# Performance work log

Measured on AMD Instinct MI355X. Metric: run time of the kernel, lower is better.

## Reference

```python
import jax, jax.numpy as jnp
import numpy as np

B, S, V, P = 16, 100, 50000, 45
WE, PE, H = 100, 50, 400
H2 = 2 * H  # bilstm output size


def _lstm(x, Wih, Whh, b):
    """Unidirectional LSTM over time. x: [B,S,D] -> h: [B,S,H]. PyTorch gate order i,f,g,o."""
    Hs = Whh.shape[1]
    def step(carry, xt):
        h, c = carry
        g = xt @ Wih.T + h @ Whh.T + b
        i, f, gg, o = jnp.split(g, 4, axis=-1)
        c = jax.nn.sigmoid(f) * c + jax.nn.sigmoid(i) * jnp.tanh(gg)
        h = jax.nn.sigmoid(o) * jnp.tanh(c)
        return (h, c), h
    Bn = x.shape[0]
    init = (jnp.zeros((Bn, Hs), x.dtype), jnp.zeros((Bn, Hs), x.dtype))
    _, hs = jax.lax.scan(step, init, jnp.swapaxes(x, 0, 1))
    return jnp.swapaxes(hs, 0, 1)


def _bilstm_layer(x, Wf_ih, Wf_hh, bf, Wb_ih, Wb_hh, bb):
    hf = _lstm(x, Wf_ih, Wf_hh, bf)
    hb = _lstm(x[:, ::-1, :], Wb_ih, Wb_hh, bb)[:, ::-1, :]
    return jnp.concatenate([hf, hb], axis=-1)


def setup_inputs() -> dict:
    key = jax.random.key(0)
    ks = jax.random.split(key, 24)
    def n(k, shape, s=0.1):
        return jax.random.normal(k, shape, jnp.float32) * s
    inp = {
        "input_tokens": jax.random.randint(ks[0], (B, S), 0, V),
        "input_pos": jax.random.randint(ks[1], (B, S), 0, P),
        "input_head": jax.random.randint(ks[2], (B, S), 0, S),
        "word_W": n(ks[3], (V, WE)),
        "pos_W": n(ks[4], (P, PE)),
        "l0f_Wih": n(ks[5], (4 * H, WE + PE)), "l0f_Whh": n(ks[6], (4 * H, H)), "l0f_b": n(ks[7], (4 * H,)),
        "l0b_Wih": n(ks[8], (4 * H, WE + PE)), "l0b_Whh": n(ks[9], (4 * H, H)), "l0b_b": n(ks[10], (4 * H,)),
        "l1f_Wih": n(ks[11], (4 * H, H2)), "l1f_Whh": n(ks[12], (4 * H, H)), "l1f_b": n(ks[13], (4 * H,)),
        "l1b_Wih": n(ks[14], (4 * H, H2)), "l1b_Whh": n(ks[15], (4 * H, H)), "l1b_b": n(ks[16], (4 * H,)),
        "ua_W": n(ks[17], (H2, H2)), "ua_b": n(ks[18], (H2,)),
        "wa_W": n(ks[19], (H2, H2)), "wa_b": n(ks[20], (H2,)),
        "va_W": n(ks[21], (H2,)),
    }
    return inp


def reference(input_tokens, input_pos, input_head, word_W, pos_W,
              l0f_Wih, l0f_Whh, l0f_b, l0b_Wih, l0b_Whh, l0b_b,
              l1f_Wih, l1f_Whh, l1f_b, l1b_Wih, l1b_Whh, l1b_b,
              ua_W, ua_b, wa_W, wa_b, va_W):
    # embeddings (dropout is identity at eval)
    x = jnp.concatenate([word_W[input_tokens], pos_W[input_pos]], axis=-1)  # [B,S,150]
    h1 = _bilstm_layer(x, l0f_Wih, l0f_Whh, l0f_b, l0b_Wih, l0b_Whh, l0b_b)   # [B,S,H2]
    out = _bilstm_layer(h1, l1f_Wih, l1f_Whh, l1f_b, l1b_Wih, l1b_Whh, l1b_b)  # [B,S,H2]

    # batched additive biaffine scoring for targets i = 1..S-1 over all source positions j
    ua = out @ ua_W.T + ua_b  # u_a(source)  [B,S,H2]
    wa = out @ wa_W.T + wa_b  # w_a(target)  [B,S,H2]
    # g[b,t,j] = v_a . tanh(ua[b,j] + wa[b,t+1])
    g = jnp.einsum('btjh,h->btj', jnp.tanh(ua[:, None, :, :] + wa[:, 1:, None, :]), va_W)  # [B,S-1,S]
    # mask: output[:, j, 0] == output[:, i, 0]  (masks self, matching torch's output.eq(target)[:,:,0])
    mask = out[:, 1:, 0][:, :, None] == out[:, :, 0][:, None, :]  # [B,S-1,S]
    g = jnp.where(mask, -10000.0, g)
    logp = jax.nn.log_softmax(g, axis=2)  # log_softmax over source positions (torch dim=1)

    # loss: sum over i of NLLLoss(mean over batch, ignore_index=-1)
    gold = input_head[:, 1:]  # [B,S-1]
    valid = (gold != -1)
    nll = -jnp.take_along_axis(logp, jnp.clip(gold, 0, S - 1)[:, :, None], axis=2)[..., 0]
    nll = nll * valid.astype(logp.dtype)
    denom = jnp.maximum(valid.sum(axis=0), 1).astype(logp.dtype)
    loss = jnp.sum(nll.sum(axis=0) / denom)

    parent_prob_table = jnp.exp(logp)  # [B,S-1,S]
    preds = jnp.argmax(parent_prob_table, axis=2)  # [B,S-1]
    return (loss, preds, parent_prob_table)
```

## Files before the change

kernel.cpp:

```cpp
#include <hip/hip_runtime.h>

#define BB 16
#define SS 100
#define HH 400
#define H2 800
#define G4 1600
#define DIN0 150
#define KP0 160

#define OFF_X0   0ULL
#define OFF_GF   240000ULL
#define OFF_GB   2800000ULL
#define OFF_H1   5360000ULL
#define OFF_OUT2 6640000ULL
#define OFF_SC   7920000ULL
#define OFF_NLL  8078400ULL
#define OFF_CNT  8080000ULL
#define OFF_EXH  8081600ULL
#define EX_U16_PER_PLANE 1331200ULL

#define PAD_X0   0ULL
#define PAD_WF   256000ULL
#define PAD_WB   512000ULL

typedef _Float16 f16x8 __attribute__((ext_vector_type(8)));
typedef float    f32x4 __attribute__((ext_vector_type(4)));

__global__ __launch_bounds__(256) void embed_pad_kernel(
    const int* __restrict__ tok, const int* __restrict__ pos,
    const float* __restrict__ wW, const float* __restrict__ pW,
    const float* __restrict__ Wf, const float* __restrict__ Wb,
    float* __restrict__ stage)
{
    int idx = blockIdx.x * 256 + threadIdx.x;
    if (idx >= 3 * 1600 * KP0) return;
    int which = idx / (1600 * KP0);
    int rem = idx % (1600 * KP0);
    int r = rem / KP0, k = rem % KP0;
    float v = 0.f;
    if (which == 0) {
        if (k < 100)       v = wW[tok[r] * 100 + k];
        else if (k < 150)  v = pW[pos[r] * 50 + (k - 100)];
        stage[PAD_X0 + (size_t)r * KP0 + k] = v;
    } else if (which == 1) {
        if (k < DIN0) v = Wf[r * DIN0 + k];
        stage[PAD_WF + (size_t)r * KP0 + k] = v;
    } else {
        if (k < DIN0) v = Wb[r * DIN0 + k];
        stage[PAD_WB + (size_t)r * KP0 + k] = v;
    }
}

static __device__ __forceinline__ void cvt_pair8(float4 a, float4 b,
                                                 f16x8& hi, f16x8& lo)
{
    float v[8] = {a.x, a.y, a.z, a.w, b.x, b.y, b.z, b.w};
#pragma unroll
    for (int i = 0; i < 8; i++) {
        _Float16 h = (_Float16)v[i];
        hi[i] = h;
        lo[i] = (_Float16)((v[i] - (float)h) * 2048.f);
    }
}

__global__ __launch_bounds__(256) void gemm_nt_mfma_dual(
    const float* __restrict__ A,
    const float* __restrict__ W0, const float* __restrict__ b0, float* __restrict__ C0,
    const float* __restrict__ W1, const float* __restrict__ b1, float* __restrict__ C1,
    int N, int K, int R)
{
    int half = gridDim.x >> 1;
    int sel = blockIdx.x >= half;
    int bx = blockIdx.x - (sel ? half : 0);
    const float* W = sel ? W1 : W0;
    const float* bias = sel ? b1 : b0;
    float* C = sel ? C1 : C0;

    int tid = threadIdx.x;
    int wv = tid >> 6, l = tid & 63;
    int lm = l & 15, lk = l >> 4;
    int rs = bx * 64 + wv * 16;
    if (rs >= R) return;
    int n0 = blockIdx.y * 64;

    const float* wrow = W + (size_t)(rs + lm) * K + lk * 8;
    const float* arow = A + (size_t)(n0 + lm) * K + lk * 8;

    f32x4 accH[4], accX[4];
#pragma unroll
    for (int ct = 0; ct < 4; ct++) {
        accH[ct] = {0.f, 0.f, 0.f, 0.f};
        accX[ct] = {0.f, 0.f, 0.f, 0.f};
    }

    int ksteps = K >> 5;
    for (int kt = 0; kt < ksteps; kt++) {
        int kb = kt << 5;
        float4 wlo4 = *(const float4*)(wrow + kb);
        float4 whi4 = *(const float4*)(wrow + kb + 4);
        f16x8 wh, wl;
        cvt_pair8(wlo4, whi4, wh, wl);
#pragma unroll
        for (int ct = 0; ct < 4; ct++) {
            const float* ap = arow + (size_t)(ct * 16) * K + kb;
            float4 aa = *(const float4*)ap;
            float4 ab = *(const float4*)(ap + 4);
            f16x8 ah, al;
            cvt_pair8(aa, ab, ah, al);
            accH[ct] = __builtin_amdgcn_mfma_f32_16x16x32_f16(wh, ah, accH[ct], 0, 0, 0);
            accX[ct] = __builtin_amdgcn_mfma_f32_16x16x32_f16(wh, al, accX[ct], 0, 0, 0);
            accX[ct] = __builtin_amdgcn_mfma_f32_16x16x32_f16(wl, ah, accX[ct], 0, 0, 0);
        }
    }

    float4 bv = *(const float4*)&bias[rs + lk * 4];
#pragma unroll
    for (int ct = 0; ct < 4; ct++) {
        f32x4 v = accH[ct] + accX[ct] * (1.f / 2048.f);
        float4 o;
        o.x = v[0] + bv.x; o.y = v[1] + bv.y; o.z = v[2] + bv.z; o.w = v[3] + bv.w;
        *(float4*)&C[(size_t)(n0 + ct * 16 + lm) * R + rs + lk * 4] = o;
    }
}

__global__ __launch_bounds__(64, 1) void lstm_layer_kernel(
    const float* __restrict__ Gf, const float* __restrict__ Gb,
    const float* __restrict__ Wf, const float* __restrict__ Wb,
    float* __restrict__ hbuf,
    int* __restrict__ cnt,
    unsigned short* __restrict__ exhi,
    unsigned short* __restrict__ exlo)
{
    const int dir = blockIdx.x / 100;
    const int wg  = blockIdx.x % 100;
    const int j0  = wg * 4;
    const float* __restrict__ G = dir ? Gb : Gf;
    const float* __restrict__ W = dir ? Wb : Wf;

    const int l   = threadIdx.x;
    const int b   = l & 15;
    const int hi4 = l >> 4;

    __shared__ __attribute__((aligned(16))) unsigned short ahi[13 * 64 * 8];
    __shared__ __attribute__((aligned(16))) unsigned short alo[13 * 64 * 8];
    __shared__ float gl[16 * 17];

    {
        const int m = b;
        const int g = m >> 2, jj = m & 3;
        const float* wrow = W + (size_t)(g * HH + j0 + jj) * HH;
        for (int kt = 0; kt < 13; kt++) {
            for (int e = 0; e < 8; e++) {
                int k = kt * 32 + hi4 * 8 + e;
                float w = (k < HH) ? wrow[k] : 0.f;
                _Float16 wh = (_Float16)w;
                _Float16 wl = (_Float16)((w - (float)wh) * 2048.f);
                ahi[(kt * 64 + l) * 8 + e] = __builtin_bit_cast(unsigned short, wh);
                alo[(kt * 64 + l) * 8 + e] = __builtin_bit_cast(unsigned short, wl);
            }
        }
    }
    __syncthreads();

    float c_reg = 0.f;
    unsigned short* exh_d = exhi + (size_t)dir * 100 * 13 * 512;
    unsigned short* exl_d = exlo + (size_t)dir * 100 * 13 * 512;

    for (int s = 0; s < SS; s++) {
        const int time = dir ? (SS - 1 - s) : s;
        f32x4 gpre = *(const f32x4*)&G[(size_t)(b * SS + time) * G4 + hi4 * HH + j0];

        f32x4 acc;
        if (s > 0) {
            int* c4 = cnt + (dir * SS + (s - 1)) * 4;
            for (int guard = 0; guard < (1 << 20); guard++) {
                int sum = 0;
                if (l == 0) {
                    sum  = __hip_atomic_load(c4 + 0, __ATOMIC_RELAXED, __HIP_MEMORY_SCOPE_AGENT);
                    sum += __hip_atomic_load(c4 + 1, __ATOMIC_RELAXED, __HIP_MEMORY_SCOPE_AGENT);
                    sum += __hip_atomic_load(c4 + 2, __ATOMIC_RELAXED, __HIP_MEMORY_SCOPE_AGENT);
                    sum += __hip_atomic_load(c4 + 3, __ATOMIC_RELAXED, __HIP_MEMORY_SCOPE_AGENT);
                }
                if (__ballot(sum >= 100) & 1ull) break;
                __builtin_amdgcn_s_sleep(1);
            }
            asm volatile("" ::: "memory");

            const f16x8* __restrict__ pbh = (const f16x8*)(exh_d + (size_t)(s - 1) * 13 * 512);
            const f16x8* __restrict__ pbl = (const f16x8*)(exl_d + (size_t)(s - 1) * 13 * 512);
            f16x8 bh[13], bl[13];
#pragma unroll
            for (int kt = 0; kt < 13; kt++) {
                bh[kt] = pbh[kt * 64 + l];
                bl[kt] = pbl[kt * 64 + l];
            }
            f32x4 aHH = gpre;
            f32x4 aHL = {0.f, 0.f, 0.f, 0.f};
            f32x4 aLH = {0.f, 0.f, 0.f, 0.f};
#pragma unroll
            for (int kt = 0; kt < 13; kt++) {
                f16x8 wh = *(const f16x8*)&ahi[(kt * 64 + l) * 8];
                f16x8 wl = *(const f16x8*)&alo[(kt * 64 + l) * 8];
                aHH = __builtin_amdgcn_mfma_f32_16x16x32_f16(wh, bh[kt], aHH, 0, 0, 0);
                aHL = __builtin_amdgcn_mfma_f32_16x16x32_f16(wh, bl[kt], aHL, 0, 0, 0);
                aLH = __builtin_amdgcn_mfma_f32_16x16x32_f16(wl, bh[kt], aLH, 0, 0, 0);
            }
            acc = aHH + (aHL + aLH) * (1.f / 2048.f);
        } else {
            acc = gpre;
        }

#pragma unroll
        for (int q = 0; q < 4; q++) gl[(4 * hi4 + q) * 17 + b] = acc[q];
        __syncthreads();

        const int jj = hi4;
        float gi = gl[( 0 + jj) * 17 + b];
        float gf = gl[( 4 + jj) * 17 + b];
        float gg = gl[( 8 + jj) * 17 + b];
        float go = gl[(12 + jj) * 17 + b];
        __syncthreads();

        float si = 1.f / (1.f + expf(-gi));
        float sf = 1.f / (1.f + expf(-gf));
        float tg = tanhf(gg);
        float so = 1.f / (1.f + expf(-go));
        float c  = sf * c_reg + si * tg;
        c_reg = c;
        float h  = so * tanhf(c);

        hbuf[(size_t)(b * SS + time) * H2 + dir * HH + j0 + jj] = h;

        if (s < SS - 1) {
            _Float16 hh = (_Float16)h;
            _Float16 hl = (_Float16)((h - (float)hh) * 2048.f);
            unsigned uh = __builtin_bit_cast(unsigned short, hh);
            unsigned ul = __builtin_bit_cast(unsigned short, hl);
            unsigned ph = uh | (((unsigned)__shfl_down((int)uh, 16)) << 16);
            unsigned pl = ul | (((unsigned)__shfl_down((int)ul, 16)) << 16);
            if ((jj & 1) == 0) {
                int k0 = j0 + jj;
                int kt = k0 >> 5, ko = k0 & 31;
                int lg = ko >> 3, e = ko & 7;
                size_t u16idx = ((size_t)(s * 13 + kt) * 64 + (lg * 16 + b)) * 8 + e;
                __hip_atomic_store((unsigned*)(exh_d + u16idx), ph,
                                   __ATOMIC_RELAXED, __HIP_MEMORY_SCOPE_AGENT);
                __hip_atomic_store((unsigned*)(exl_d + u16idx), pl,
                                   __ATOMIC_RELAXED, __HIP_MEMORY_SCOPE_AGENT);
            }
            asm volatile("s_waitcnt vmcnt(0)" ::: "memory");
            if (l == 0)
                __hip_atomic_fetch_add(cnt + (dir * SS + s) * 4 + (wg & 3), 1,
                                       __ATOMIC_RELAXED, __HIP_MEMORY_SCOPE_AGENT);
        }
    }
}

#define ITILE 11
__global__ __launch_bounds__(256) void attn_scores_kernel(
    const float* __restrict__ ua, const float* __restrict__ wa,
    const float* __restrict__ va, float* __restrict__ scores)
{
    int b  = blockIdx.x / 9;
    int i0 = (blockIdx.x % 9) * ITILE;
    int tid = threadIdx.x;
    __shared__ float ua_t[100][101];
    __shared__ float wa_t[ITILE][102];
    __shared__ float sacc[ITILE][101];
    __shared__ float va_t[100];

    for (int p = tid; p < ITILE * 101; p += 256) ((float*)sacc)[p] = 0.f;

    for (int ht = 0; ht < 8; ht++) {
        int h0 = ht * 100;
        __syncthreads();
        for (int p = tid; p < 100 * 100; p += 256) {
            int j = p / 100, hh = p % 100;
            ua_t[j][hh] = ua[(size_t)(b * SS + j) * H2 + h0 + hh];
        }
        for (int p = tid; p < ITILE * 100; p += 256) {
            int il = p / 100, hh = p % 100;
            wa_t[il][hh] = wa[(size_t)(b * SS + i0 + il + 1) * H2 + h0 + hh];
        }
        if (tid < 100) va_t[tid] = va[h0 + tid];
        __syncthreads();
        for (int p = tid; p < ITILE * 100; p += 256) {
            int il = p / 100, j = p % 100;
            float acc = 0.f;
#pragma unroll 4
            for (int hh = 0; hh < 100; hh++) {
                float x = ua_t[j][hh] + wa_t[il][hh];
                float z = __expf(2.f * x);
                float th = 1.f - 2.f * __builtin_amdgcn_rcpf(z + 1.f);
                acc = fmaf(th, va_t[hh], acc);
            }
            sacc[il][j] += acc;
        }
    }
    __syncthreads();
    for (int p = tid; p < ITILE * 100; p += 256) {
        int il = p / 100, j = p % 100;
        scores[(size_t)(b * 99 + i0 + il) * 100 + j] = sacc[il][j];
    }
}

__global__ __launch_bounds__(128) void attn_softmax_kernel(
    const float* __restrict__ scores, const float* __restrict__ out2,
    const int* __restrict__ head, float* __restrict__ outb,
    float* __restrict__ nll)
{
    int bi = blockIdx.x;
    int b = bi / 99, i = bi % 99;
    int j = threadIdx.x;
    __shared__ float sv[128];
    __shared__ int   si[128];
    __shared__ float red[128];

    float h_t = out2[(size_t)(b * SS + i + 1) * H2];
    float sj = -1e30f;
    if (j < 100) {
        sj = scores[(size_t)bi * 100 + j];
        float h_j = out2[(size_t)(b * SS + j) * H2];
        if (h_j == h_t) sj = -10000.0f;
    }
    sv[j] = sj; si[j] = j;
    __syncthreads();
    for (int off = 64; off >= 1; off >>= 1) {
        if (j < off) {
            float o = sv[j + off]; int oi = si[j + off];
            if (o > sv[j] || (o == sv[j] && oi < si[j])) { sv[j] = o; si[j] = oi; }
        }
        __syncthreads();
    }
    float m = sv[0]; int amax = si[0];
    __syncthreads();
    float e = (j < 100) ? __expf(sj - m) : 0.f;
    red[j] = e;
    __syncthreads();
    for (int off = 64; off >= 1; off >>= 1) {
        if (j < off) red[j] += red[j + off];
        __syncthreads();
    }
    float sum = red[0];
    float inv = 1.f / sum;
    if (j < 100) outb[1 + 1584 + (size_t)bi * 100 + j] = e * inv;
    if (j == 0) {
        outb[1 + bi] = (float)amax;
        int gold = head[b * SS + i + 1];
        bool valid = (gold != -1);
        int gc = gold < 0 ? 0 : (gold > 99 ? 99 : gold);
        float sgc = scores[(size_t)bi * 100 + gc];
        float hgc = out2[(size_t)(b * SS + gc) * H2];
        if (hgc == h_t) sgc = -10000.0f;
        nll[bi] = valid ? -(sgc - m - logf(sum)) : 0.f;
    }
}

__global__ __launch_bounds__(128) void loss_kernel(
    const float* __restrict__ nll, const int* __restrict__ head,
    float* __restrict__ outb)
{
    __shared__ float red[128];
    int tid = threadIdx.x;
    float contrib = 0.f;
    if (tid < 99) {
        int i = tid;
        float tot = 0.f; int cv = 0;
        for (int b = 0; b < BB; b++) {
            tot += nll[b * 99 + i];
            cv += (head[b * SS + i + 1] != -1) ? 1 : 0;
        }
        int denom = cv > 0 ? cv : 1;
        contrib = tot / (float)denom;
    }
    red[tid] = contrib;
    __syncthreads();
    for (int off = 64; off >= 1; off >>= 1) {
        if (tid < off) red[tid] += red[tid + off];
        __syncthreads();
    }
    if (tid == 0) outb[0] = red[0];
}

extern "C" void kernel_launch(void* const* d_in, const int* in_sizes, int n_in,
                              void* d_out, int out_size, void* d_ws, size_t ws_size,
                              hipStream_t stream) {
    const int*   tok     = (const int*)d_in[0];
    const int*   pos     = (const int*)d_in[1];
    const int*   head    = (const int*)d_in[2];
    const float* word_W  = (const float*)d_in[3];
    const float* pos_W   = (const float*)d_in[4];
    const float* l0f_Wih = (const float*)d_in[5];
    const float* l0f_Whh = (const float*)d_in[6];
    const float* l0f_b   = (const float*)d_in[7];
    const float* l0b_Wih = (const float*)d_in[8];
    const float* l0b_Whh = (const float*)d_in[9];
    const float* l0b_b   = (const float*)d_in[10];
    const float* l1f_Wih = (const float*)d_in[11];
    const float* l1f_Whh = (const float*)d_in[12];
    const float* l1f_b   = (const float*)d_in[13];
    const float* l1b_Wih = (const float*)d_in[14];
    const float* l1b_Whh = (const float*)d_in[15];
    const float* l1b_b   = (const float*)d_in[16];
    const float* ua_W    = (const float*)d_in[17];
    const float* ua_b    = (const float*)d_in[18];
    const float* wa_W    = (const float*)d_in[19];
    const float* wa_b    = (const float*)d_in[20];
    const float* va_W    = (const float*)d_in[21];

    float* ws   = (float*)d_ws;
    float* gf   = ws + OFF_GF;
    float* gb   = ws + OFF_GB;
    float* h1   = ws + OFF_H1;
    float* out2 = ws + OFF_OUT2;
    float* sc   = ws + OFF_SC;
    float* nllb = ws + OFF_NLL;
    int*   cnt  = (int*)(ws + OFF_CNT);
    unsigned short* exhi = (unsigned short*)(ws + OFF_EXH);
    unsigned short* exlo = exhi + EX_U16_PER_PLANE;
    float* outf = (float*)d_out;

    hipMemsetAsync(cnt, 0, 1600 * sizeof(int) + 2 * EX_U16_PER_PLANE * sizeof(unsigned short), stream);

    embed_pad_kernel<<<dim3((3 * 1600 * KP0 + 255) / 256), 256, 0, stream>>>(
        tok, pos, word_W, pos_W, l0f_Wih, l0b_Wih, out2);

    float* x0p = out2 + PAD_X0;
    float* wfp = out2 + PAD_WF;
    float* wbp = out2 + PAD_WB;

    gemm_nt_mfma_dual<<<dim3(50, 25), 256, 0, stream>>>(
        x0p, wfp, l0f_b, gf, wbp, l0b_b, gb, 1600, KP0, G4);
    lstm_layer_kernel<<<dim3(200), 64, 0, stream>>>(
        gf, gb, l0f_Whh, l0b_Whh, h1, cnt, exhi, exlo);
    gemm_nt_mfma_dual<<<dim3(50, 25), 256, 0, stream>>>(
        h1, l1f_Wih, l1f_b, gf, l1b_Wih, l1b_b, gb, 1600, H2, G4);
    lstm_layer_kernel<<<dim3(200), 64, 0, stream>>>(
        gf, gb, l1f_Whh, l1b_Whh, out2, cnt + 800, exhi, exlo);
    gemm_nt_mfma_dual<<<dim3(26, 25), 256, 0, stream>>>(
        out2, ua_W, ua_b, gf, wa_W, wa_b, gb, 1600, H2, H2);
    attn_scores_kernel<<<dim3(16 * 9), 256, 0, stream>>>(gf, gb, va_W, sc);
    attn_softmax_kernel<<<dim3(1584), 128, 0, stream>>>(sc, out2, head, outf, nllb);
    loss_kernel<<<dim3(1), 128, 0, stream>>>(nllb, head, outf);
}
```

Measured before the change: 1.471 ms.

## Replace LSTM step counters with poison-value flags embedded in exchanged data

Removes the per-step atomic counters and the vmcnt(0) drain before signalling. Each workgroup now spins directly on the exchanged fp16 hidden-state buffers, which are pre-filled with 0xFFFFFFFF sentinels and re-poisoned by the layer-1 input GEMM. Readiness is detected when no 32-bit word still holds the sentinel. This cuts one round-trip of synchronisation latency per timestep, at the cost of polling the full data on every spin and relying on the sentinel never matching a real fp16 pair. The hbuf store is also moved after the exchange stores, so the exchange leaves the workgroup sooner.

```diff
diff --git a/kernel.cpp b/kernel.cpp
--- a/kernel.cpp
+++ b/kernel.cpp
@@ -8,14 +8,12 @@
 #define DIN0 150
 #define KP0 160
 
-#define OFF_X0   0ULL
 #define OFF_GF   240000ULL
 #define OFF_GB   2800000ULL
 #define OFF_H1   5360000ULL
 #define OFF_OUT2 6640000ULL
 #define OFF_SC   7920000ULL
 #define OFF_NLL  8078400ULL
-#define OFF_CNT  8080000ULL
 #define OFF_EXH  8081600ULL
 #define EX_U16_PER_PLANE 1331200ULL
 
@@ -25,6 +23,16 @@
 
 typedef _Float16 f16x8 __attribute__((ext_vector_type(8)));
 typedef float    f32x4 __attribute__((ext_vector_type(4)));
+typedef unsigned long long u64x2 __attribute__((ext_vector_type(2)));
+
+static __device__ __forceinline__ unsigned chkp(unsigned long long q) {
+    return ((unsigned)q == 0xFFFFFFFFu) | ((unsigned)(q >> 32) == 0xFFFFFFFFu);
+}
+static __device__ __forceinline__ unsigned long long sanq(unsigned long long q) {
+    if ((unsigned)q == 0xFFFFFFFFu)         q &= 0xFFFFFFFF00000000ull;
+    if ((unsigned)(q >> 32) == 0xFFFFFFFFu) q &= 0x00000000FFFFFFFFull;
+    return q;
+}
 
 __global__ __launch_bounds__(256) void embed_pad_kernel(
     const int* __restrict__ tok, const int* __restrict__ pos,
@@ -67,8 +75,15 @@
     const float* __restrict__ A,
     const float* __restrict__ W0, const float* __restrict__ b0, float* __restrict__ C0,
     const float* __restrict__ W1, const float* __restrict__ b1, float* __restrict__ C1,
-    int N, int K, int R)
-{
+    int N, int K, int R,
+    unsigned int* __restrict__ poison, int poison_words)
+{
+    if (poison) {
+        int nthreads = gridDim.x * gridDim.y * 256;
+        int gtid = (blockIdx.y * gridDim.x + blockIdx.x) * 256 + threadIdx.x;
+        for (int i = gtid; i < poison_words; i += nthreads) poison[i] = 0xFFFFFFFFu;
+    }
+
     int half = gridDim.x >> 1;
     int sel = blockIdx.x >= half;
     int bx = blockIdx.x - (sel ? half : 0);
@@ -127,7 +142,6 @@
     const float* __restrict__ Gf, const float* __restrict__ Gb,
     const float* __restrict__ Wf, const float* __restrict__ Wb,
     float* __restrict__ hbuf,
-    int* __restrict__ cnt,
     unsigned short* __restrict__ exhi,
     unsigned short* __restrict__ exlo)
 {
@@ -165,6 +179,7 @@
     float c_reg = 0.f;
     unsigned short* exh_d = exhi + (size_t)dir * 100 * 13 * 512;
     unsigned short* exl_d = exlo + (size_t)dir * 100 * 13 * 512;
+    const int pad_lane = (hi4 >= 2);
 
     for (int s = 0; s < SS; s++) {
         const int time = dir ? (SS - 1 - s) : s;
@@ -172,38 +187,62 @@
 
         f32x4 acc;
         if (s > 0) {
-            int* c4 = cnt + (dir * SS + (s - 1)) * 4;
-            for (int guard = 0; guard < (1 << 20); guard++) {
-                int sum = 0;
-                if (l == 0) {
-                    sum  = __hip_atomic_load(c4 + 0, __ATOMIC_RELAXED, __HIP_MEMORY_SCOPE_AGENT);
-                    sum += __hip_atomic_load(c4 + 1, __ATOMIC_RELAXED, __HIP_MEMORY_SCOPE_AGENT);
-                    sum += __hip_atomic_load(c4 + 2, __ATOMIC_RELAXED, __HIP_MEMORY_SCOPE_AGENT);
-                    sum += __hip_atomic_load(c4 + 3, __ATOMIC_RELAXED, __HIP_MEMORY_SCOPE_AGENT);
+            const unsigned long long* pbh =
+                (const unsigned long long*)(exh_d + (size_t)(s - 1) * 13 * 512);
+            const unsigned long long* pbl =
+                (const unsigned long long*)(exl_d + (size_t)(s - 1) * 13 * 512);
+            u64x2 vh2[13], vl2[13];
+            vh2[12] = {0ull, 0ull};
+            vl2[12] = {0ull, 0ull};
+            unsigned bad = 1;
+            for (int guard = 0; guard < (1 << 13); guard++) {
+                bad = 0;
+#pragma unroll
+                for (int kt = 0; kt < 12; kt++) {
+                    size_t q = (size_t)(kt * 64 + l) * 2;
+                    vh2[kt][0] = __hip_atomic_load(pbh + q,     __ATOMIC_RELAXED, __HIP_MEMORY_SCOPE_AGENT);
+                    vh2[kt][1] = __hip_atomic_load(pbh + q + 1, __ATOMIC_RELAXED, __HIP_MEMORY_SCOPE_AGENT);
+                    vl2[kt][0] = __hip_atomic_load(pbl + q,     __ATOMIC_RELAXED, __HIP_MEMORY_SCOPE_AGENT);
+                    vl2[kt][1] = __hip_atomic_load(pbl + q + 1, __ATOMIC_RELAXED, __HIP_MEMORY_SCOPE_AGENT);
                 }
-                if (__ballot(sum >= 100) & 1ull) break;
-                __builtin_amdgcn_s_sleep(1);
+                if (!pad_lane) {
+                    size_t q = (size_t)(12 * 64 + l) * 2;
+                    vh2[12][0] = __hip_atomic_load(pbh + q,     __ATOMIC_RELAXED, __HIP_MEMORY_SCOPE_AGENT);
+                    vh2[12][1] = __hip_atomic_load(pbh + q + 1, __ATOMIC_RELAXED, __HIP_MEMORY_SCOPE_AGENT);
+                    vl2[12][0] = __hip_atomic_load(pbl + q,     __ATOMIC_RELAXED, __HIP_MEMORY_SCOPE_AGENT);
+                    vl2[12][1] = __hip_atomic_load(pbl + q + 1, __ATOMIC_RELAXED, __HIP_MEMORY_SCOPE_AGENT);
+                    bad |= chkp(vh2[12][0]) | chkp(vh2[12][1])
+                         | chkp(vl2[12][0]) | chkp(vl2[12][1]);
+                }
+#pragma unroll
+                for (int kt = 0; kt < 12; kt++) {
+                    bad |= chkp(vh2[kt][0]) | chkp(vh2[kt][1])
+                         | chkp(vl2[kt][0]) | chkp(vl2[kt][1]);
+                }
+                if (__ballot(bad != 0) == 0ull) break;
+                __builtin_amdgcn_s_sleep(2);
+            }
+            if (bad) {
+#pragma unroll
+                for (int kt = 0; kt < 13; kt++) {
+                    vh2[kt][0] = sanq(vh2[kt][0]); vh2[kt][1] = sanq(vh2[kt][1]);
+                    vl2[kt][0] = sanq(vl2[kt][0]); vl2[kt][1] = sanq(vl2[kt][1]);
+                }
             }
             asm volatile("" ::: "memory");
 
-            const f16x8* __restrict__ pbh = (const f16x8*)(exh_d + (size_t)(s - 1) * 13 * 512);
-            const f16x8* __restrict__ pbl = (const f16x8*)(exl_d + (size_t)(s - 1) * 13 * 512);
-            f16x8 bh[13], bl[13];
-#pragma unroll
-            for (int kt = 0; kt < 13; kt++) {
-                bh[kt] = pbh[kt * 64 + l];
-                bl[kt] = pbl[kt * 64 + l];
-            }
             f32x4 aHH = gpre;
             f32x4 aHL = {0.f, 0.f, 0.f, 0.f};
             f32x4 aLH = {0.f, 0.f, 0.f, 0.f};
 #pragma unroll
             for (int kt = 0; kt < 13; kt++) {
+                f16x8 bhv = __builtin_bit_cast(f16x8, vh2[kt]);
+                f16x8 blv = __builtin_bit_cast(f16x8, vl2[kt]);
                 f16x8 wh = *(const f16x8*)&ahi[(kt * 64 + l) * 8];
                 f16x8 wl = *(const f16x8*)&alo[(kt * 64 + l) * 8];
-                aHH = __builtin_amdgcn_mfma_f32_16x16x32_f16(wh, bh[kt], aHH, 0, 0, 0);
-                aHL = __builtin_amdgcn_mfma_f32_16x16x32_f16(wh, bl[kt], aHL, 0, 0, 0);
-                aLH = __builtin_amdgcn_mfma_f32_16x16x32_f16(wl, bh[kt], aLH, 0, 0, 0);
+                aHH = __builtin_amdgcn_mfma_f32_16x16x32_f16(wh, bhv, aHH, 0, 0, 0);
+                aHL = __builtin_amdgcn_mfma_f32_16x16x32_f16(wh, blv, aHL, 0, 0, 0);
+                aLH = __builtin_amdgcn_mfma_f32_16x16x32_f16(wl, bhv, aLH, 0, 0, 0);
             }
             acc = aHH + (aHL + aLH) * (1.f / 2048.f);
         } else {
@@ -228,8 +267,6 @@
         float c  = sf * c_reg + si * tg;
         c_reg = c;
         float h  = so * tanhf(c);
-
-        hbuf[(size_t)(b * SS + time) * H2 + dir * HH + j0 + jj] = h;
 
         if (s < SS - 1) {
             _Float16 hh = (_Float16)h;
@@ -248,11 +285,9 @@
                 __hip_atomic_store((unsigned*)(exl_d + u16idx), pl,
                                    __ATOMIC_RELAXED, __HIP_MEMORY_SCOPE_AGENT);
             }
-            asm volatile("s_waitcnt vmcnt(0)" ::: "memory");
-            if (l == 0)
-                __hip_atomic_fetch_add(cnt + (dir * SS + s) * 4 + (wg & 3), 1,
-                                       __ATOMIC_RELAXED, __HIP_MEMORY_SCOPE_AGENT);
-        }
+        }
+
+        hbuf[(size_t)(b * SS + time) * H2 + dir * HH + j0 + jj] = h;
     }
 }
 
@@ -415,12 +450,11 @@
     float* out2 = ws + OFF_OUT2;
     float* sc   = ws + OFF_SC;
     float* nllb = ws + OFF_NLL;
-    int*   cnt  = (int*)(ws + OFF_CNT);
     unsigned short* exhi = (unsigned short*)(ws + OFF_EXH);
     unsigned short* exlo = exhi + EX_U16_PER_PLANE;
     float* outf = (float*)d_out;
 
-    hipMemsetAsync(cnt, 0, 1600 * sizeof(int) + 2 * EX_U16_PER_PLANE * sizeof(unsigned short), stream);
+    hipMemsetAsync(exhi, 0xFF, 2 * EX_U16_PER_PLANE * sizeof(unsigned short), stream);
 
     embed_pad_kernel<<<dim3((3 * 1600 * KP0 + 255) / 256), 256, 0, stream>>>(
         tok, pos, word_W, pos_W, l0f_Wih, l0b_Wih, out2);
@@ -430,15 +464,16 @@
     float* wbp = out2 + PAD_WB;
 
     gemm_nt_mfma_dual<<<dim3(50, 25), 256, 0, stream>>>(
-        x0p, wfp, l0f_b, gf, wbp, l0b_b, gb, 1600, KP0, G4);
+        x0p, wfp, l0f_b, gf, wbp, l0b_b, gb, 1600, KP0, G4, nullptr, 0);
     lstm_layer_kernel<<<dim3(200), 64, 0, stream>>>(
-        gf, gb, l0f_Whh, l0b_Whh, h1, cnt, exhi, exlo);
+        gf, gb, l0f_Whh, l0b_Whh, h1, exhi, exlo);
     gemm_nt_mfma_dual<<<dim3(50, 25), 256, 0, stream>>>(
-        h1, l1f_Wih, l1f_b, gf, l1b_Wih, l1b_b, gb, 1600, H2, G4);
+        h1, l1f_Wih, l1f_b, gf, l1b_Wih, l1b_b, gb, 1600, H2, G4,
+        (unsigned int*)exhi, (int)EX_U16_PER_PLANE);
     lstm_layer_kernel<<<dim3(200), 64, 0, stream>>>(
-        gf, gb, l1f_Whh, l1b_Whh, out2, cnt + 800, exhi, exlo);
+        gf, gb, l1f_Whh, l1b_Whh, out2, exhi, exlo);
     gemm_nt_mfma_dual<<<dim3(26, 25), 256, 0, stream>>>(
-        out2, ua_W, ua_b, gf, wa_W, wa_b, gb, 1600, H2, H2);
+        out2, ua_W, ua_b, gf, wa_W, wa_b, gb, 1600, H2, H2, nullptr, 0);
     attn_scores_kernel<<<dim3(16 * 9), 256, 0, stream>>>(gf, gb, va_W, sc);
     attn_softmax_kernel<<<dim3(1584), 128, 0, stream>>>(sc, out2, head, outf, nllb);
     loss_kernel<<<dim3(1), 128, 0, stream>>>(nllb, head, outf);
```

Result: faster. 1.440 ms (-2.0%).
